# Performance work log

Measured on AMD Instinct MI355X. Metric: run time of the kernel, lower is better.

Reference implementation:

```python
import jax, jax.numpy as jnp
import numpy as np

B, T, H = 2, 1024, 4096
HK, HV, DK, DV = 8, 32, 64, 64
VPK = HV // HK            # value heads per key head = 4
KEY_DIM = HK * DK         # 512
VAL_DIM = HV * DV         # 2048
CONV_DIM = 2 * KEY_DIM + VAL_DIM  # 3072
KSZ = 4
EPS = 1e-5
L2_EPS = 1e-6


def _l2norm(x):
    return x * jax.lax.rsqrt(jnp.sum(x * x, axis=-1, keepdims=True) + L2_EPS)


def setup_inputs() -> dict:
    key = jax.random.key(0)
    ks = jax.random.split(key, 8)
    s = 0.02
    return {
        "hidden_states": jax.random.normal(ks[0], (B, T, H), jnp.float32),
        "W_qkvz": jax.random.normal(ks[1], (H, 2 * KEY_DIM + 2 * VAL_DIM), jnp.float32) * s,
        "W_ba": jax.random.normal(ks[2], (H, 2 * HV), jnp.float32) * s,
        "conv_w": jax.random.normal(ks[3], (CONV_DIM, KSZ), jnp.float32) * 0.1,
        "dt_bias": jnp.ones((HV,), jnp.float32),
        "A_log": jnp.log(jax.random.uniform(ks[4], (HV,), jnp.float32, 1.0, 16.0)),
        "norm_w": jnp.ones((DV,), jnp.float32),
        "W_out": jax.random.normal(ks[5], (VAL_DIM, H), jnp.float32) * s,
    }


def _forward(hidden_states, W_qkvz, W_ba, conv_w, dt_bias, A_log, norm_w, W_out):
    # --- projections ---
    qkvz = hidden_states @ W_qkvz                       # [B,T,5120]
    ba = hidden_states @ W_ba                           # [B,T,64]
    # fix_query_key_value_ordering: per key head [q(Dk), k(Dk), v(vpk*Dv), z(vpk*Dv)]
    qkvz = qkvz.reshape(B, T, HK, 2 * DK + 2 * VPK * DV)
    q = qkvz[..., :DK]                                  # [B,T,HK,DK]
    k = qkvz[..., DK:2 * DK]
    v = qkvz[..., 2 * DK:2 * DK + VPK * DV].reshape(B, T, HV, DV)
    z = qkvz[..., 2 * DK + VPK * DV:].reshape(B, T, HV, DV)
    ba = ba.reshape(B, T, HK, 2 * VPK)
    b = ba[..., :VPK].reshape(B, T, HV)
    a = ba[..., VPK:].reshape(B, T, HV)

    # --- causal depthwise conv over concatenated qkv, then silu ---
    mixed = jnp.concatenate(
        [q.reshape(B, T, KEY_DIM), k.reshape(B, T, KEY_DIM), v.reshape(B, T, VAL_DIM)], axis=-1)
    padded = jnp.pad(mixed, ((0, 0), (KSZ - 1, 0), (0, 0)))
    conv = sum(padded[:, j:j + T, :] * conv_w[:, j] for j in range(KSZ))
    conv = jax.nn.silu(conv)
    q = conv[..., :KEY_DIM].reshape(B, T, HK, DK)
    k = conv[..., KEY_DIM:2 * KEY_DIM].reshape(B, T, HK, DK)
    v = conv[..., 2 * KEY_DIM:].reshape(B, T, HV, DV)

    # --- fused GDN gating: g = -exp(A_log)*softplus(a+dt_bias), beta = sigmoid(b) ---
    g = -jnp.exp(A_log) * jax.nn.softplus(a + dt_bias)  # [B,T,HV]
    beta = jax.nn.sigmoid(b)                            # [B,T,HV]

    # --- q/k l2 norm + scale, broadcast key heads to value heads ---
    q = _l2norm(q) * (DK ** -0.5)
    k = _l2norm(k)
    q = jnp.repeat(q, VPK, axis=2)                      # [B,T,HV,DK]
    k = jnp.repeat(k, VPK, axis=2)

    # --- gated delta-rule recurrence over time ---
    def step(S, inp):
        qt, kt, vt, gt, bt = inp                        # qt/kt [B,HV,DK], vt [B,HV,DV]
        S = S * jnp.exp(gt)[..., None, None]            # decay
        pred = jnp.einsum('bhk,bhkv->bhv', kt, S)
        delta = (vt - pred) * bt[..., None]
        S = S + jnp.einsum('bhk,bhv->bhkv', kt, delta)
        o = jnp.einsum('bhk,bhkv->bhv', qt, S)
        return S, o

    xs = (q.transpose(1, 0, 2, 3), k.transpose(1, 0, 2, 3), v.transpose(1, 0, 2, 3),
          g.transpose(1, 0, 2), beta.transpose(1, 0, 2))
    S0 = jnp.zeros((B, HV, DK, DV), q.dtype)
    _, o = jax.lax.scan(step, S0, xs)                   # [T,B,HV,DV]
    o = o.transpose(1, 0, 2, 3)                         # [B,T,HV,DV]

    # --- gated RMSNorm (norm before gate) + out projection ---
    o_n = o * jax.lax.rsqrt(jnp.mean(o * o, axis=-1, keepdims=True) + EPS) * norm_w
    o_n = o_n * jax.nn.silu(z)
    return o_n.reshape(B, T, VAL_DIM) @ W_out           # [B,T,H]


def reference(hidden_states, W_qkvz, W_ba, conv_w, dt_bias, A_log, norm_w, W_out):
    return _forward(hidden_states, W_qkvz, W_ba, conv_w, dt_bias, A_log, norm_w, W_out)
```

## Files before the change

kernel.cpp:

```cpp
#include <hip/hip_runtime.h>
#include <hip/hip_bf16.h>
#include <cstdint>
#include <cstddef>


typedef __attribute__((ext_vector_type(8))) short short8;
typedef __attribute__((ext_vector_type(4))) float f32x4;

__device__ __forceinline__ short f2bf(float f) {
  union { float f; unsigned u; } x; x.f = f;
  unsigned r = x.u + 0x7fffu + ((x.u >> 16) & 1u);
  return (short)(r >> 16);
}

__device__ __forceinline__ void gl_lds16(const short* g, short* l) {
  __builtin_amdgcn_global_load_lds(
      (const __attribute__((address_space(1))) void*)g,
      (__attribute__((address_space(3))) void*)l, 16, 0, 0);
}

__global__ __launch_bounds__(256) void to_bf16_kernel(const float* __restrict__ x,
                                                      short* __restrict__ y) {
  int i = blockIdx.x * 256 + threadIdx.x;
  float4 v = ((const float4*)x)[i];
  ushort4 r;
  r.x = (unsigned short)f2bf(v.x);
  r.y = (unsigned short)f2bf(v.y);
  r.z = (unsigned short)f2bf(v.z);
  r.w = (unsigned short)f2bf(v.w);
  ((ushort4*)y)[i] = r;
}

__global__ __launch_bounds__(256) void transpose_w1(const float* __restrict__ Wq,
                                                    const float* __restrict__ Wba,
                                                    short* __restrict__ Wt) {
  __shared__ float tile[32][33];
  int n0 = blockIdx.x * 32;
  int k0 = blockIdx.y * 32;
  int t = threadIdx.x;
  int r = t >> 5;
  int c = t & 31;
#pragma unroll
  for (int i = 0; i < 4; ++i) {
    int kl = r + i * 8;
    int n = n0 + c;
    float v = 0.f;
    if (n < 5120) v = Wq[(size_t)(k0 + kl) * 5120 + n];
    else if (n < 5184) v = Wba[(size_t)(k0 + kl) * 64 + (n - 5120)];
    tile[kl][c] = v;
  }
  __syncthreads();
#pragma unroll
  for (int i = 0; i < 4; ++i) {
    int nl = r + i * 8;
    int kl = c;
    Wt[(size_t)(n0 + nl) * 4096 + k0 + kl] = f2bf(tile[kl][nl]);
  }
}

__global__ __launch_bounds__(256) void transpose_w2(const float* __restrict__ W,
                                                    short* __restrict__ Wt) {
  __shared__ float tile[32][33];
  int n0 = blockIdx.x * 32;
  int k0 = blockIdx.y * 32;
  int t = threadIdx.x;
  int r = t >> 5;
  int c = t & 31;
#pragma unroll
  for (int i = 0; i < 4; ++i) {
    int kl = r + i * 8;
    tile[kl][c] = W[(size_t)(k0 + kl) * 4096 + n0 + c];
  }
  __syncthreads();
#pragma unroll
  for (int i = 0; i < 4; ++i) {
    int nl = r + i * 8;
    int kl = c;
    Wt[(size_t)(n0 + nl) * 2048 + k0 + kl] = f2bf(tile[kl][nl]);
  }
}

template <bool GUARD_N>
__global__ __launch_bounds__(256) void gemm128p(const short* __restrict__ A,
                                                const short* __restrict__ Bt,
                                                float* __restrict__ C,
                                                int N, int K, int MT) {
  __shared__ __align__(16) short As[3 * 4096];
  __shared__ __align__(16) short Bs[3 * 4096];
  const int tid = threadIdx.x;
  const int w = tid >> 6, lane = tid & 63;
  const int wm = w >> 1, wn = w & 1;

  const int nwg = gridDim.x;
  const int bid = blockIdx.x;
  const int swz = (bid & 7) * (nwg >> 3) + (bid >> 3);
  const int m0 = (swz % MT) * 128;
  const int n0 = (swz / MT) * 128;

  const int p0 = w * 64 + lane;
  const int rp0 = p0 >> 3, q0 = p0 & 7;
  const int mm0 = q0 ^ (rp0 & 7);
  const int srow = rp0 * 2 + (mm0 >> 2);
  const int scol = (mm0 & 3) << 3;
  const short* Ag = A + (size_t)(m0 + srow) * K + scol;
  const short* Bg = Bt + (size_t)(n0 + srow) * K + scol;
  const size_t rstep = (size_t)64 * K;

  const int fr = lane & 15;
  const int s = lane >> 4;
  int aoff[4], boff[4];
#pragma unroll
  for (int i = 0; i < 4; ++i) {
    int row = wm * 64 + i * 16 + fr;
    int rp = row >> 1;
    int q = (((row & 1) << 2) | s) ^ (rp & 7);
    aoff[i] = (rp * 8 + q) * 8;
  }
#pragma unroll
  for (int j = 0; j < 4; ++j) {
    int row = wn * 64 + j * 16 + fr;
    int rp = row >> 1;
    int q = (((row & 1) << 2) | s) ^ (rp & 7);
    boff[j] = (rp * 8 + q) * 8;
  }

  f32x4 acc[4][4];
#pragma unroll
  for (int i = 0; i < 4; ++i)
#pragma unroll
    for (int j = 0; j < 4; ++j) acc[i][j] = (f32x4){0.f, 0.f, 0.f, 0.f};

  const int NKT = K >> 5;

#define STAGE_A(kt, bb)                                                \
  { const short* g = Ag + (size_t)(kt) * 32;                           \
    gl_lds16(g,         &As[(bb) * 4096 + w * 512]);                   \
    gl_lds16(g + rstep, &As[(bb) * 4096 + 2048 + w * 512]); }
#define STAGE_B(kt, bb)                                                \
  { const short* g = Bg + (size_t)(kt) * 32;                           \
    gl_lds16(g,         &Bs[(bb) * 4096 + w * 512]);                   \
    gl_lds16(g + rstep, &Bs[(bb) * 4096 + 2048 + w * 512]); }

  STAGE_A(0, 0); STAGE_B(0, 0);
  STAGE_A(1, 1); STAGE_B(1, 1);
  asm volatile("s_waitcnt vmcnt(4)" ::: "memory");
  __builtin_amdgcn_s_barrier();
  __builtin_amdgcn_sched_barrier(0);

  int bi = 0;
  for (int kt = 0; kt < NKT; ++kt) {
    int bi2 = bi - 1; if (bi2 < 0) bi2 = 2;
    const short* Ab = &As[bi * 4096];
    const short* Bb = &Bs[bi * 4096];
    short8 af[2], bf[4];
#pragma unroll
    for (int i = 0; i < 2; ++i) af[i] = *(const short8*)&Ab[aoff[i]];
#pragma unroll
    for (int j = 0; j < 4; ++j) bf[j] = *(const short8*)&Bb[boff[j]];
    if (kt + 2 < NKT) STAGE_A(kt + 2, bi2);
    __builtin_amdgcn_s_barrier();
    asm volatile("s_waitcnt lgkmcnt(0)" ::: "memory");
    __builtin_amdgcn_sched_barrier(0);
    __builtin_amdgcn_s_setprio(1);
#pragma unroll
    for (int i = 0; i < 2; ++i)
#pragma unroll
      for (int j = 0; j < 4; ++j)
        acc[i][j] = __builtin_amdgcn_mfma_f32_16x16x32_bf16(af[i], bf[j], acc[i][j], 0, 0, 0);
    __builtin_amdgcn_s_setprio(0);
    __builtin_amdgcn_sched_barrier(0);
#pragma unroll
    for (int i = 0; i < 2; ++i) af[i] = *(const short8*)&Ab[aoff[i + 2]];
    if (kt + 2 < NKT) STAGE_B(kt + 2, bi2);
    if (kt < NKT - 2) { asm volatile("s_waitcnt vmcnt(4)" ::: "memory"); }
    else              { asm volatile("s_waitcnt vmcnt(0)" ::: "memory"); }
    __builtin_amdgcn_s_barrier();
    asm volatile("s_waitcnt lgkmcnt(0)" ::: "memory");
    __builtin_amdgcn_sched_barrier(0);
    __builtin_amdgcn_s_setprio(1);
#pragma unroll
    for (int i = 0; i < 2; ++i)
#pragma unroll
      for (int j = 0; j < 4; ++j)
        acc[i + 2][j] = __builtin_amdgcn_mfma_f32_16x16x32_bf16(af[i], bf[j], acc[i + 2][j], 0, 0, 0);
    __builtin_amdgcn_s_setprio(0);
    __builtin_amdgcn_sched_barrier(0);
    __builtin_amdgcn_s_barrier();
    ++bi; if (bi == 3) bi = 0;
  }
#undef STAGE_A
#undef STAGE_B

  const int rbase = (lane >> 4) << 2;
#pragma unroll
  for (int i = 0; i < 4; ++i) {
#pragma unroll
    for (int j = 0; j < 4; ++j) {
      int col = n0 + wn * 64 + j * 16 + fr;
      if (GUARD_N && col >= N) continue;
      int row = m0 + wm * 64 + i * 16 + rbase;
#pragma unroll
      for (int r = 0; r < 4; ++r)
        C[(size_t)(row + r) * N + col] = acc[i][j][r];
    }
  }
}

__global__ __launch_bounds__(256) void conv_kernel(const float* __restrict__ qkvz,
                                                   const float* __restrict__ conv_w,
                                                   float* __restrict__ mix) {
  __shared__ float sq[1024];
  __shared__ float scale[16];
  int bt = blockIdx.x;
  int t = bt & 1023;
  int tid = threadIdx.x;
  for (int c = tid; c < 3072; c += 256) {
    int col;
    if (c < 512) {
      col = (c >> 6) * 640 + (c & 63);
    } else if (c < 1024) {
      int c2 = c - 512;
      col = (c2 >> 6) * 640 + 64 + (c2 & 63);
    } else {
      int c3 = c - 1024;
      int hv = c3 >> 6;
      col = (hv >> 2) * 640 + 128 + (hv & 3) * 64 + (c3 & 63);
    }
    float acc = 0.f;
#pragma unroll
    for (int j = 0; j < 4; ++j) {
      int tt = t - 3 + j;
      if (tt >= 0) acc += qkvz[(size_t)(bt - 3 + j) * 5184 + col] * conv_w[c * 4 + j];
    }
    float sv = acc / (1.f + __expf(-acc));
    if (c < 1024)
      sq[c] = sv;
    else
      mix[(size_t)bt * 3072 + c] = sv;
  }
  __syncthreads();
  int g = tid >> 4, l = tid & 15;
  float p = 0.f;
#pragma unroll
  for (int i = 0; i < 4; ++i) {
    float v = sq[g * 64 + l * 4 + i];
    p += v * v;
  }
  p += __shfl_xor(p, 1);
  p += __shfl_xor(p, 2);
  p += __shfl_xor(p, 4);
  p += __shfl_xor(p, 8);
  if (l == 0) scale[g] = rsqrtf(p + 1e-6f);
  __syncthreads();
  for (int c = tid; c < 1024; c += 256) {
    float s = scale[c >> 6] * ((c < 512) ? 0.125f : 1.f);
    mix[(size_t)bt * 3072 + c] = sq[c] * s;
  }
}

__global__ __launch_bounds__(256) void gate_kernel(const float* __restrict__ qkvz,
                                                   const float* __restrict__ dt_bias,
                                                   const float* __restrict__ A_log,
                                                   float* __restrict__ gb,
                                                   float* __restrict__ beta) {
  int i = blockIdx.x * 256 + threadIdx.x;
  int hv = i & 31;
  int bt = i >> 5;
  int hk = hv >> 2, vp = hv & 3;
  const float* row = qkvz + (size_t)bt * 5184 + 5120 + hk * 8;
  float bv = row[vp];
  float av = row[4 + vp];
  float x = av + dt_bias[hv];
  float sp = (x > 20.f) ? x : log1pf(expf(x));
  gb[i] = -expf(A_log[hv]) * sp;
  beta[i] = 1.f / (1.f + expf(-bv));
}

__global__ __launch_bounds__(256) void precompute_kernel(
    const float* __restrict__ mix, const float* __restrict__ gbuf,
    const float* __restrict__ betab, float* __restrict__ Wbuf,
    float* __restrict__ Pbuf, float* __restrict__ Rbuf, float* __restrict__ cbuf) {
  __shared__ float Kt[64][68];
  __shared__ float Vb[64][68];
  __shared__ float AM[64][68];
  __shared__ float Mm[64][68];
  __shared__ float Tb[16][17];
  __shared__ float cs[64], bb[64];

  const int u = blockIdx.x;
  const int chunk = u & 15, hv = (u >> 4) & 31, b = u >> 9;
  const int hk = hv >> 2;
  const int t0g = b * 1024 + chunk * 64;
  const int tid = threadIdx.x;
  const int tr = tid >> 2, q4 = tid & 3;

  {
    const float* mrow = mix + (size_t)(t0g + tr) * 3072;
#pragma unroll
    for (int e = 0; e < 4; ++e) {
      int c0 = q4 * 16 + e * 4;
      float4 kv = *(const float4*)(mrow + 512 + hk * 64 + c0);
      Kt[c0 + 0][tr] = kv.x; Kt[c0 + 1][tr] = kv.y;
      Kt[c0 + 2][tr] = kv.z; Kt[c0 + 3][tr] = kv.w;
      *(float4*)&Vb[tr][c0] = *(const float4*)(mrow + 1024 + hv * 64 + c0);
    }
  }
  if (tid < 64) {
    cs[tid] = gbuf[(size_t)(t0g + tid) * 32 + hv];
    bb[tid] = betab[(size_t)(t0g + tid) * 32 + hv];
  }
  __syncthreads();
  for (int off = 1; off < 64; off <<= 1) {
    float v = 0.f;
    if (tid < 64 && tid >= off) v = cs[tid - off];
    __syncthreads();
    if (tid < 64) cs[tid] += v;
    __syncthreads();
  }
  if (tid < 64) cbuf[(size_t)u * 64 + tid] = cs[tid];

  {
    float acc[16];
#pragma unroll
    for (int i = 0; i < 16; ++i) acc[i] = 0.f;
    for (int d = 0; d < 64; ++d) {
      float kv = Kt[d][tr];
#pragma unroll
      for (int e = 0; e < 4; ++e) {
        float4 ks = *(const float4*)&Kt[d][q4 * 16 + e * 4];
        acc[e * 4 + 0] += kv * ks.x; acc[e * 4 + 1] += kv * ks.y;
        acc[e * 4 + 2] += kv * ks.z; acc[e * 4 + 3] += kv * ks.w;
      }
    }
    float bt_ = bb[tr], ct_ = cs[tr];
#pragma unroll
    for (int j = 0; j < 16; ++j) {
      int s = q4 * 16 + j;
      AM[tr][s] = (s < tr) ? bt_ * acc[j] * __expf(ct_ - cs[s]) : 0.f;
    }
  }
  __syncthreads();

  for (int i = tid; i < 64 * 68; i += 256) (&Mm[0][0])[i] = 0.f;
  __syncthreads();
  if (tid < 64) {
    int blk = tid >> 4, j = tid & 15, base = blk * 16;
    Mm[base][base + j] = (j == 0) ? 1.f : 0.f;
    for (int r = 1; r < 16; ++r) {
      float sum = 0.f;
      for (int s = 0; s < r; ++s) sum += AM[base + r][base + s] * Mm[base + s][base + j];
      Mm[base + r][base + j] = ((r == j) ? 1.f : 0.f) - sum;
    }
  }
  __syncthreads();
  for (int d = 1; d < 4; ++d) {
    for (int j = 0; j + d < 4; ++j) {
      int i = j + d;
      int r = tid >> 4, c = tid & 15;
      float tsum = 0.f;
      for (int kb = j; kb < i; ++kb)
        for (int uu = 0; uu < 16; ++uu)
          tsum += AM[i * 16 + r][kb * 16 + uu] * Mm[kb * 16 + uu][j * 16 + c];
      Tb[r][c] = tsum;
      __syncthreads();
      float msum = 0.f;
      for (int uu = 0; uu < 16; ++uu)
        msum += Mm[i * 16 + r][i * 16 + uu] * Tb[uu][c];
      __syncthreads();
      Mm[i * 16 + r][j * 16 + c] = -msum;
      __syncthreads();
    }
  }

  {
    const float* mrow = mix + (size_t)(t0g + tr) * 3072 + hk * 64;
#pragma unroll
    for (int e = 0; e < 4; ++e) {
      int c0 = q4 * 16 + e * 4;
      float4 qv = *(const float4*)(mrow + c0);
      AM[c0 + 0][tr] = qv.x; AM[c0 + 1][tr] = qv.y;
      AM[c0 + 2][tr] = qv.z; AM[c0 + 3][tr] = qv.w;
    }
  }
  __syncthreads();

  {
    float acc[16];
#pragma unroll
    for (int i = 0; i < 16; ++i) acc[i] = 0.f;
    for (int d = 0; d < 64; ++d) {
      float qv = AM[d][tr];
#pragma unroll
      for (int e = 0; e < 4; ++e) {
        float4 ks = *(const float4*)&Kt[d][q4 * 16 + e * 4];
        acc[e * 4 + 0] += qv * ks.x; acc[e * 4 + 1] += qv * ks.y;
        acc[e * 4 + 2] += qv * ks.z; acc[e * 4 + 3] += qv * ks.w;
      }
    }
    float ct_ = cs[tr];
#pragma unroll
    for (int e = 0; e < 4; ++e) {
      int s0 = q4 * 16 + e * 4;
      float4 pv;
      pv.x = (s0 + 0 <= tr) ? acc[e * 4 + 0] * __expf(ct_ - cs[s0 + 0]) : 0.f;
      pv.y = (s0 + 1 <= tr) ? acc[e * 4 + 1] * __expf(ct_ - cs[s0 + 1]) : 0.f;
      pv.z = (s0 + 2 <= tr) ? acc[e * 4 + 2] * __expf(ct_ - cs[s0 + 2]) : 0.f;
      pv.w = (s0 + 3 <= tr) ? acc[e * 4 + 3] * __expf(ct_ - cs[s0 + 3]) : 0.f;
      *(float4*)&Pbuf[(size_t)u * 4096 + tr * 64 + s0] = pv;
    }
  }
  __syncthreads();

  {
    float vals[16];
#pragma unroll
    for (int j = 0; j < 16; ++j) vals[j] = Kt[q4 * 16 + j][tr];
    float sc = bb[tr] * __expf(cs[tr]);
    __syncthreads();
#pragma unroll
    for (int j = 0; j < 16; ++j) Kt[tr][q4 * 16 + j] = vals[j] * sc;
  }
  __syncthreads();

  {
    float acc[16];
#pragma unroll
    for (int i = 0; i < 16; ++i) acc[i] = 0.f;
    for (int s = 0; s < 64; ++s) {
      float m = Mm[tr][s];
#pragma unroll
      for (int e = 0; e < 4; ++e) {
        float4 kk = *(const float4*)&Kt[s][q4 * 16 + e * 4];
        acc[e * 4 + 0] += m * kk.x; acc[e * 4 + 1] += m * kk.y;
        acc[e * 4 + 2] += m * kk.z; acc[e * 4 + 3] += m * kk.w;
      }
    }
#pragma unroll
    for (int e = 0; e < 4; ++e) {
      float4 wv = {acc[e * 4 + 0], acc[e * 4 + 1], acc[e * 4 + 2], acc[e * 4 + 3]};
      *(float4*)&Wbuf[(size_t)u * 4096 + tr * 64 + q4 * 16 + e * 4] = wv;
    }
  }
  {
    float acc[16];
#pragma unroll
    for (int i = 0; i < 16; ++i) acc[i] = 0.f;
    for (int s = 0; s < 64; ++s) {
      float m = Mm[tr][s] * bb[s];
#pragma unroll
      for (int e = 0; e < 4; ++e) {
        float4 vv = *(const float4*)&Vb[s][q4 * 16 + e * 4];
        acc[e * 4 + 0] += m * vv.x; acc[e * 4 + 1] += m * vv.y;
        acc[e * 4 + 2] += m * vv.z; acc[e * 4 + 3] += m * vv.w;
      }
    }
#pragma unroll
    for (int e = 0; e < 4; ++e) {
      float4 rv = {acc[e * 4 + 0], acc[e * 4 + 1], acc[e * 4 + 2], acc[e * 4 + 3]};
      *(float4*)&Rbuf[(size_t)u * 4096 + tr * 64 + q4 * 16 + e * 4] = rv;
    }
  }
}

__global__ __launch_bounds__(512) void chunk_scan_kernel(
    const float* __restrict__ mix, const float* __restrict__ Wbuf,
    const float* __restrict__ Pbuf, const float* __restrict__ Rbuf,
    const float* __restrict__ cbuf, float* __restrict__ o) {
  __shared__ float Wb[64][68], Pb[64][68], Qh[64][68], Kt[64][68];
  __shared__ float St[16][68], Dt[16][68];
  __shared__ float cs[64];

  const int bid = blockIdx.x;
  const int vs = bid & 3, hv = (bid >> 2) & 31, b = bid >> 7;
  const int hk = hv >> 2;
  const int bh = b * 32 + hv;
  const int ubase = bh * 16;
  const int tid = threadIdx.x;
  const int tr = tid >> 3, q8 = tid & 7;
  const int c0 = q8 * 2, c1 = q8 * 2 + 1;

  for (int i = tid; i < 16 * 68; i += 512) (&St[0][0])[i] = 0.f;

  float4 WN[2], PN[2], KN[2], QN[2];
  float2 RN;
  float cN = 0.f;
  float e63c = 1.f;

#define ISSUE_LOADS(c)                                                          \
  {                                                                             \
    size_t uu = (size_t)(ubase + (c));                                          \
    _Pragma("unroll") for (int i = 0; i < 2; ++i) {                             \
      WN[i] = ((const float4*)(Wbuf + uu * 4096))[tid + 512 * i];               \
      PN[i] = ((const float4*)(Pbuf + uu * 4096))[tid + 512 * i];               \
    }                                                                           \
    const float* mrow = mix + (size_t)(b * 1024 + (c) * 64 + tr) * 3072;        \
    _Pragma("unroll") for (int e = 0; e < 2; ++e) {                             \
      KN[e] = *(const float4*)(mrow + 512 + hk * 64 + q8 * 8 + e * 4);          \
      QN[e] = *(const float4*)(mrow + hk * 64 + q8 * 8 + e * 4);                \
    }                                                                           \
    RN = *(const float2*)(Rbuf + uu * 4096 + tr * 64 + vs * 16 + q8 * 2);       \
    if (tid < 64) cN = cbuf[uu * 64 + tid];                                     \
  }

#define COMMIT()                                                                \
  {                                                                             \
    _Pragma("unroll") for (int i = 0; i < 2; ++i) {                             \
      int flat = (tid + 512 * i) * 4;                                           \
      int rr = flat >> 6, cc = flat & 63;                                       \
      *(float4*)&Wb[rr][cc] = WN[i];                                            \
      *(float4*)&Pb[rr][cc] = PN[i];                                            \
    }                                                                           \
    if (tid < 64) cs[tid] = cN;                                                 \
    __syncthreads();                                                            \
    float csv = cs[tr], cs63 = cs[63];                                          \
    float sQv = __expf(csv), sKv = __expf(cs63 - csv);                          \
    e63c = __expf(cs63);                                                        \
    float4 qa, qb;                                                              \
    qa.x = QN[0].x * sQv; qa.y = QN[0].y * sQv;                                 \
    qa.z = QN[0].z * sQv; qa.w = QN[0].w * sQv;                                 \
    qb.x = QN[1].x * sQv; qb.y = QN[1].y * sQv;                                 \
    qb.z = QN[1].z * sQv; qb.w = QN[1].w * sQv;                                 \
    *(float4*)&Qh[tr][q8 * 8] = qa;                                             \
    *(float4*)&Qh[tr][q8 * 8 + 4] = qb;                                         \
    Kt[q8 * 8 + 0][tr] = KN[0].x * sKv;                                         \
    Kt[q8 * 8 + 1][tr] = KN[0].y * sKv;                                         \
    Kt[q8 * 8 + 2][tr] = KN[0].z * sKv;                                         \
    Kt[q8 * 8 + 3][tr] = KN[0].w * sKv;                                         \
    Kt[q8 * 8 + 4][tr] = KN[1].x * sKv;                                         \
    Kt[q8 * 8 + 5][tr] = KN[1].y * sKv;                                         \
    Kt[q8 * 8 + 6][tr] = KN[1].z * sKv;                                         \
    Kt[q8 * 8 + 7][tr] = KN[1].w * sKv;                                         \
  }

  ISSUE_LOADS(0);
  COMMIT();
  float2 Rv = RN;

  for (int c = 0; c < 16; ++c) {
    if (c < 15) ISSUE_LOADS(c + 1);
    float2 acc = Rv;
#pragma unroll 4
    for (int k = 0; k < 64; k += 4) {
      float4 w4 = *(const float4*)&Wb[tr][k];
      float4 sa = *(const float4*)&St[c0][k];
      float4 sb = *(const float4*)&St[c1][k];
      acc.x -= w4.x * sa.x + w4.y * sa.y + w4.z * sa.z + w4.w * sa.w;
      acc.y -= w4.x * sb.x + w4.y * sb.y + w4.z * sb.z + w4.w * sb.w;
    }
    Dt[c0][tr] = acc.x;
    Dt[c1][tr] = acc.y;
    __syncthreads();
    {
      float2 ao = {0.f, 0.f};
#pragma unroll 4
      for (int i = 0; i < 64; i += 4) {
        float4 p4 = *(const float4*)&Pb[tr][i];
        float4 q4 = *(const float4*)&Qh[tr][i];
        float4 da = *(const float4*)&Dt[c0][i];
        float4 db = *(const float4*)&Dt[c1][i];
        float4 sa = *(const float4*)&St[c0][i];
        float4 sb = *(const float4*)&St[c1][i];
        ao.x += p4.x * da.x + p4.y * da.y + p4.z * da.z + p4.w * da.w
              + q4.x * sa.x + q4.y * sa.y + q4.z * sa.z + q4.w * sa.w;
        ao.y += p4.x * db.x + p4.y * db.y + p4.z * db.z + p4.w * db.w
              + q4.x * sb.x + q4.y * sb.y + q4.z * sb.z + q4.w * sb.w;
      }
      *(float2*)&o[((size_t)(bh * 4 + vs) * 1024 + c * 64 + tr) * 16 + q8 * 2] = ao;
    }
    __syncthreads();
    {
      float sx = St[c0][tr] * e63c;
      float sy = St[c1][tr] * e63c;
#pragma unroll 4
      for (int t = 0; t < 64; t += 4) {
        float4 k4 = *(const float4*)&Kt[tr][t];
        float4 da = *(const float4*)&Dt[c0][t];
        float4 db = *(const float4*)&Dt[c1][t];
        sx += k4.x * da.x + k4.y * da.y + k4.z * da.z + k4.w * da.w;
        sy += k4.x * db.x + k4.y * db.y + k4.z * db.z + k4.w * db.w;
      }
      St[c0][tr] = sx;
      St[c1][tr] = sy;
    }
    if (c < 15) {
      COMMIT();
      Rv = RN;
    }
  }
#undef ISSUE_LOADS
#undef COMMIT
}

__global__ __launch_bounds__(256) void rms_gate_kernel(const float* __restrict__ o,
                                                       const float* __restrict__ qkvz,
                                                       const float* __restrict__ norm_w,
                                                       short* __restrict__ on) {
  int bid = blockIdx.x;
  int bh = bid >> 8;
  int tg = bid & 255;
  int b = bh >> 5, hv = bh & 31;
  int t = tg * 4 + (threadIdx.x >> 6);
  int d = threadIdx.x & 63;
  int bt = b * 1024 + t;
  int hk = hv >> 2, vp = hv & 3;
  float x = o[((size_t)(bh * 4 + (d >> 4)) * 1024 + t) * 16 + (d & 15)];
  float ss = x * x;
  ss += __shfl_xor(ss, 1);
  ss += __shfl_xor(ss, 2);
  ss += __shfl_xor(ss, 4);
  ss += __shfl_xor(ss, 8);
  ss += __shfl_xor(ss, 16);
  ss += __shfl_xor(ss, 32);
  float sc = rsqrtf(ss * (1.f / 64.f) + 1e-5f);
  float z = qkvz[(size_t)bt * 5184 + hk * 640 + 384 + vp * 64 + d];
  float val = x * sc * norm_w[d] * (z / (1.f + __expf(-z)));
  on[((size_t)bt * 32 + hv) * 64 + d] = f2bf(val);
}

extern "C" void kernel_launch(void* const* d_in, const int* in_sizes, int n_in,
                              void* d_out, int out_size, void* d_ws, size_t ws_size,
                              hipStream_t stream) {
  const float* hidden = (const float*)d_in[0];
  const float* W_qkvz = (const float*)d_in[1];
  const float* W_ba = (const float*)d_in[2];
  const float* conv_w = (const float*)d_in[3];
  const float* dt_bias = (const float*)d_in[4];
  const float* A_log = (const float*)d_in[5];
  const float* norm_w = (const float*)d_in[6];
  const float* W_out = (const float*)d_in[7];
  float* out = (float*)d_out;

  char* ws = (char*)d_ws;
  short* A_bf = (short*)(ws + 0);
  short* Wt1 = (short*)(ws + 16777216);
  short* Wt2 = (short*)(ws + 59768832);
  float* qkvz = (float*)(ws + 76546048);
  float* mix = (float*)(ws + 119013376);
  float* gbuf = (float*)(ws + 144179200);
  float* beta = (float*)(ws + 144441344);
  float* o = (float*)(ws + 144703488);
  short* on = (short*)(ws + 161480704);
  float* Wbuf = (float*)(ws + 169869312);
  float* Pbuf = (float*)(ws + 186646528);
  float* Rbuf = (float*)(ws + 203423744);
  float* cbuf = (float*)(ws + 220200960);

  to_bf16_kernel<<<8192, 256, 0, stream>>>(hidden, A_bf);
  transpose_w1<<<dim3(164, 128), 256, 0, stream>>>(W_qkvz, W_ba, Wt1);
  transpose_w2<<<dim3(128, 64), 256, 0, stream>>>(W_out, Wt2);
  gemm128p<true><<<656, 256, 0, stream>>>(A_bf, Wt1, qkvz, 5184, 4096, 16);
  conv_kernel<<<2048, 256, 0, stream>>>(qkvz, conv_w, mix);
  gate_kernel<<<256, 256, 0, stream>>>(qkvz, dt_bias, A_log, gbuf, beta);
  precompute_kernel<<<1024, 256, 0, stream>>>(mix, gbuf, beta, Wbuf, Pbuf, Rbuf, cbuf);
  chunk_scan_kernel<<<256, 512, 0, stream>>>(mix, Wbuf, Pbuf, Rbuf, cbuf, o);
  rms_gate_kernel<<<16384, 256, 0, stream>>>(o, qkvz, norm_w, on);
  gemm128p<false><<<512, 256, 0, stream>>>(on, Wt2, out, 4096, 2048, 16);
}
```

Before: 562.6 us.

## Double chunk-scan threads to one output element per thread and merge phases

The chunk scan kernel now launches 1024 threads per block, so each thread owns one (row, value-column) element instead of two. The output computation and state-update dot products are merged into one loop, which removes a barrier per chunk at the cost of buffering the new state before a sync. This shortens the per-thread serial work in the latency-bound recurrence. In exchange it raises register pressure under the larger launch bound and adds LDS traffic per thread.

```diff
diff --git a/kernel.cpp b/kernel.cpp
--- a/kernel.cpp
+++ b/kernel.cpp
@@ -462,7 +462,7 @@
   }
 }
 
-__global__ __launch_bounds__(512) void chunk_scan_kernel(
+__global__ __launch_bounds__(1024) void chunk_scan_kernel(
     const float* __restrict__ mix, const float* __restrict__ Wbuf,
     const float* __restrict__ Pbuf, const float* __restrict__ Rbuf,
     const float* __restrict__ cbuf, float* __restrict__ o) {
@@ -476,111 +476,85 @@
   const int bh = b * 32 + hv;
   const int ubase = bh * 16;
   const int tid = threadIdx.x;
-  const int tr = tid >> 3, q8 = tid & 7;
-  const int c0 = q8 * 2, c1 = q8 * 2 + 1;
-
-  for (int i = tid; i < 16 * 68; i += 512) (&St[0][0])[i] = 0.f;
-
-  float4 WN[2], PN[2], KN[2], QN[2];
-  float2 RN;
-  float cN = 0.f;
+  const int tr = tid >> 4, cc = tid & 15;
+
+  if (tid < 16 * 68) (&St[0][0])[tid] = 0.f;
+  St[cc][tr] = 0.f;
+
+  float4 WN, PN, KN, QN;
+  float RN = 0.f, cN = 0.f;
   float e63c = 1.f;
 
-#define ISSUE_LOADS(c)                                                          \
+#define ISSUE_LOADS(ch)                                                         \
   {                                                                             \
-    size_t uu = (size_t)(ubase + (c));                                          \
-    _Pragma("unroll") for (int i = 0; i < 2; ++i) {                             \
-      WN[i] = ((const float4*)(Wbuf + uu * 4096))[tid + 512 * i];               \
-      PN[i] = ((const float4*)(Pbuf + uu * 4096))[tid + 512 * i];               \
-    }                                                                           \
-    const float* mrow = mix + (size_t)(b * 1024 + (c) * 64 + tr) * 3072;        \
-    _Pragma("unroll") for (int e = 0; e < 2; ++e) {                             \
-      KN[e] = *(const float4*)(mrow + 512 + hk * 64 + q8 * 8 + e * 4);          \
-      QN[e] = *(const float4*)(mrow + hk * 64 + q8 * 8 + e * 4);                \
-    }                                                                           \
-    RN = *(const float2*)(Rbuf + uu * 4096 + tr * 64 + vs * 16 + q8 * 2);       \
+    size_t uu = (size_t)(ubase + (ch));                                         \
+    WN = ((const float4*)(Wbuf + uu * 4096))[tid];                              \
+    PN = ((const float4*)(Pbuf + uu * 4096))[tid];                              \
+    const float* mrow = mix + (size_t)(b * 1024 + (ch) * 64 + tr) * 3072;       \
+    KN = *(const float4*)(mrow + 512 + hk * 64 + cc * 4);                       \
+    QN = *(const float4*)(mrow + hk * 64 + cc * 4);                             \
+    RN = Rbuf[uu * 4096 + tr * 64 + vs * 16 + cc];                              \
     if (tid < 64) cN = cbuf[uu * 64 + tid];                                     \
   }
 
 #define COMMIT()                                                                \
   {                                                                             \
-    _Pragma("unroll") for (int i = 0; i < 2; ++i) {                             \
-      int flat = (tid + 512 * i) * 4;                                           \
-      int rr = flat >> 6, cc = flat & 63;                                       \
-      *(float4*)&Wb[rr][cc] = WN[i];                                            \
-      *(float4*)&Pb[rr][cc] = PN[i];                                            \
-    }                                                                           \
+    *(float4*)&Wb[tr][cc * 4] = WN;                                             \
+    *(float4*)&Pb[tr][cc * 4] = PN;                                             \
     if (tid < 64) cs[tid] = cN;                                                 \
     __syncthreads();                                                            \
     float csv = cs[tr], cs63 = cs[63];                                          \
     float sQv = __expf(csv), sKv = __expf(cs63 - csv);                          \
     e63c = __expf(cs63);                                                        \
-    float4 qa, qb;                                                              \
-    qa.x = QN[0].x * sQv; qa.y = QN[0].y * sQv;                                 \
-    qa.z = QN[0].z * sQv; qa.w = QN[0].w * sQv;                                 \
-    qb.x = QN[1].x * sQv; qb.y = QN[1].y * sQv;                                 \
-    qb.z = QN[1].z * sQv; qb.w = QN[1].w * sQv;                                 \
-    *(float4*)&Qh[tr][q8 * 8] = qa;                                             \
-    *(float4*)&Qh[tr][q8 * 8 + 4] = qb;                                         \
-    Kt[q8 * 8 + 0][tr] = KN[0].x * sKv;                                         \
-    Kt[q8 * 8 + 1][tr] = KN[0].y * sKv;                                         \
-    Kt[q8 * 8 + 2][tr] = KN[0].z * sKv;                                         \
-    Kt[q8 * 8 + 3][tr] = KN[0].w * sKv;                                         \
-    Kt[q8 * 8 + 4][tr] = KN[1].x * sKv;                                         \
-    Kt[q8 * 8 + 5][tr] = KN[1].y * sKv;                                         \
-    Kt[q8 * 8 + 6][tr] = KN[1].z * sKv;                                         \
-    Kt[q8 * 8 + 7][tr] = KN[1].w * sKv;                                         \
+    float4 qa;                                                                  \
+    qa.x = QN.x * sQv; qa.y = QN.y * sQv;                                       \
+    qa.z = QN.z * sQv; qa.w = QN.w * sQv;                                       \
+    *(float4*)&Qh[tr][cc * 4] = qa;                                             \
+    Kt[cc * 4 + 0][tr] = KN.x * sKv;                                            \
+    Kt[cc * 4 + 1][tr] = KN.y * sKv;                                            \
+    Kt[cc * 4 + 2][tr] = KN.z * sKv;                                            \
+    Kt[cc * 4 + 3][tr] = KN.w * sKv;                                            \
   }
 
   ISSUE_LOADS(0);
+  __syncthreads();
   COMMIT();
-  float2 Rv = RN;
+  float Rv = RN;
 
   for (int c = 0; c < 16; ++c) {
     if (c < 15) ISSUE_LOADS(c + 1);
-    float2 acc = Rv;
-#pragma unroll 4
-    for (int k = 0; k < 64; k += 4) {
-      float4 w4 = *(const float4*)&Wb[tr][k];
-      float4 sa = *(const float4*)&St[c0][k];
-      float4 sb = *(const float4*)&St[c1][k];
-      acc.x -= w4.x * sa.x + w4.y * sa.y + w4.z * sa.z + w4.w * sa.w;
-      acc.y -= w4.x * sb.x + w4.y * sb.y + w4.z * sb.z + w4.w * sb.w;
-    }
-    Dt[c0][tr] = acc.x;
-    Dt[c1][tr] = acc.y;
+    float a0 = 0.f, a1 = 0.f;
+#pragma unroll
+    for (int k = 0; k < 8; ++k) {
+      float4 w4 = *(const float4*)&Wb[tr][k * 4];
+      float4 s4 = *(const float4*)&St[cc][k * 4];
+      a0 += w4.x * s4.x + w4.y * s4.y + w4.z * s4.z + w4.w * s4.w;
+    }
+#pragma unroll
+    for (int k = 8; k < 16; ++k) {
+      float4 w4 = *(const float4*)&Wb[tr][k * 4];
+      float4 s4 = *(const float4*)&St[cc][k * 4];
+      a1 += w4.x * s4.x + w4.y * s4.y + w4.z * s4.z + w4.w * s4.w;
+    }
+    Dt[cc][tr] = Rv - a0 - a1;
     __syncthreads();
     {
-      float2 ao = {0.f, 0.f};
-#pragma unroll 4
-      for (int i = 0; i < 64; i += 4) {
-        float4 p4 = *(const float4*)&Pb[tr][i];
-        float4 q4 = *(const float4*)&Qh[tr][i];
-        float4 da = *(const float4*)&Dt[c0][i];
-        float4 db = *(const float4*)&Dt[c1][i];
-        float4 sa = *(const float4*)&St[c0][i];
-        float4 sb = *(const float4*)&St[c1][i];
-        ao.x += p4.x * da.x + p4.y * da.y + p4.z * da.z + p4.w * da.w
-              + q4.x * sa.x + q4.y * sa.y + q4.z * sa.z + q4.w * sa.w;
-        ao.y += p4.x * db.x + p4.y * db.y + p4.z * db.z + p4.w * db.w
-              + q4.x * sb.x + q4.y * sb.y + q4.z * sb.z + q4.w * sb.w;
+      float op = 0.f, oq = 0.f, sn = 0.f;
+#pragma unroll
+      for (int i = 0; i < 16; ++i) {
+        float4 p4 = *(const float4*)&Pb[tr][i * 4];
+        float4 q4 = *(const float4*)&Qh[tr][i * 4];
+        float4 k4 = *(const float4*)&Kt[tr][i * 4];
+        float4 d4 = *(const float4*)&Dt[cc][i * 4];
+        float4 s4 = *(const float4*)&St[cc][i * 4];
+        op += p4.x * d4.x + p4.y * d4.y + p4.z * d4.z + p4.w * d4.w;
+        oq += q4.x * s4.x + q4.y * s4.y + q4.z * s4.z + q4.w * s4.w;
+        sn += k4.x * d4.x + k4.y * d4.y + k4.z * d4.z + k4.w * d4.w;
       }
-      *(float2*)&o[((size_t)(bh * 4 + vs) * 1024 + c * 64 + tr) * 16 + q8 * 2] = ao;
-    }
-    __syncthreads();
-    {
-      float sx = St[c0][tr] * e63c;
-      float sy = St[c1][tr] * e63c;
-#pragma unroll 4
-      for (int t = 0; t < 64; t += 4) {
-        float4 k4 = *(const float4*)&Kt[tr][t];
-        float4 da = *(const float4*)&Dt[c0][t];
-        float4 db = *(const float4*)&Dt[c1][t];
-        sx += k4.x * da.x + k4.y * da.y + k4.z * da.z + k4.w * da.w;
-        sy += k4.x * db.x + k4.y * db.y + k4.z * db.z + k4.w * db.w;
-      }
-      St[c0][tr] = sx;
-      St[c1][tr] = sy;
+      o[((size_t)(bh * 4 + vs) * 1024 + c * 64 + tr) * 16 + cc] = op + oq;
+      float snew = St[cc][tr] * e63c + sn;
+      __syncthreads();
+      St[cc][tr] = snew;
     }
     if (c < 15) {
       COMMIT();
@@ -652,7 +626,7 @@
   conv_kernel<<<2048, 256, 0, stream>>>(qkvz, conv_w, mix);
   gate_kernel<<<256, 256, 0, stream>>>(qkvz, dt_bias, A_log, gbuf, beta);
   precompute_kernel<<<1024, 256, 0, stream>>>(mix, gbuf, beta, Wbuf, Pbuf, Rbuf, cbuf);
-  chunk_scan_kernel<<<256, 512, 0, stream>>>(mix, Wbuf, Pbuf, Rbuf, cbuf, o);
+  chunk_scan_kernel<<<256, 1024, 0, stream>>>(mix, Wbuf, Pbuf, Rbuf, cbuf, o);
   rms_gate_kernel<<<16384, 256, 0, stream>>>(o, qkvz, norm_w, on);
   gemm128p<false><<<512, 256, 0, stream>>>(on, Wt2, out, 4096, 2048, 16);
 }
```

Measured after the change: 564.7 us. No clear change (+0.4%).
